# Performance work log

Measured on AMD Instinct MI355X. Metric: run time of the kernel, lower is better.

## Reference

```python
import jax, jax.numpy as jnp
import numpy as np

IN_DIM = 1024
FF = 512
OUT = 128
TEMP = 1.0  # temperature=1 passed in __init__
EPS = 1e-5  # BatchNorm3d eps


def make_pe(n, d):
    # PositionalEncoding table, rows 0..n-1
    pos = jnp.arange(n, dtype=jnp.float32)[:, None]
    div = jnp.exp(jnp.arange(0, d, 2, dtype=jnp.float32) * (-np.log(10000.0) / d))
    ang = pos * div  # [n, d/2]
    return jnp.stack([jnp.sin(ang), jnp.cos(ang)], axis=-1).reshape(n, d)


def _nonlocal(x, kw, qw, vw, ow, ob, g, beta):
    # x: [B, C, T, H, W]; 1x1x1 convs are channel matmuls
    B, C, T, H, W = x.shape
    K = jnp.einsum('bcthw,fc->bfthw', x, kw).reshape(B, FF, -1)
    Q = jnp.einsum('bcthw,fc->bfthw', x, qw).reshape(B, FF, -1)
    V = jnp.einsum('bcthw,fc->bfthw', x, vw).reshape(B, FF, -1)
    KQ = jnp.einsum('bcn,bcm->bnm', K, Q)  # K^T Q over channels -> [B,N,N]
    attn = jax.nn.softmax(KQ / TEMP, axis=2)
    # torch: sum_j V[b,c,n] * attn[b,n,j]  == V * attn.sum(axis=2)
    Vo = (V * attn.sum(axis=2)[:, None, :]).reshape(B, FF, T, H, W)
    o = jnp.einsum('bfthw,of->bothw', Vo, ow) + ob[None, :, None, None, None]
    y = x + jax.nn.relu(o)
    # BatchNorm3d, training-mode batch statistics over (B,T,H,W)
    m = y.mean(axis=(0, 2, 3, 4))
    v = y.var(axis=(0, 2, 3, 4))
    inv = jax.lax.rsqrt(v + EPS)
    return ((y - m[None, :, None, None, None]) * inv[None, :, None, None, None]
            * g[None, :, None, None, None] + beta[None, :, None, None, None])


def _convt2(x, w, b):
    # ConvTranspose2d(kernel=2, stride=2): each input pixel emits a 2x2 block
    B, C, H, W = x.shape
    y = jnp.einsum('bchw,cokl->bohkwl', x, w).reshape(B, w.shape[1], 2 * H, 2 * W)
    return y + b[None, :, None, None]


def setup_inputs() -> dict:
    key = jax.random.key(0)
    ks = jax.random.split(key, 32)
    n = lambda k, s, sc: jax.random.normal(k, s, dtype=jnp.float32) * sc
    d = {
        'context': n(ks[0], (4, 4, IN_DIM, 16, 16), 1.0),
        'frame': n(ks[1], (4, 6, IN_DIM, 8, 8), 1.0),
    }
    i = 2
    for l in (0, 1):
        d[f'nl{l}_kw'] = n(ks[i], (FF, IN_DIM), IN_DIM ** -0.5); i += 1
        d[f'nl{l}_qw'] = n(ks[i], (FF, IN_DIM), IN_DIM ** -0.5); i += 1
        d[f'nl{l}_vw'] = n(ks[i], (FF, IN_DIM), IN_DIM ** -0.5); i += 1
        d[f'nl{l}_ow'] = n(ks[i], (IN_DIM, FF), FF ** -0.5); i += 1
        d[f'nl{l}_ob'] = n(ks[i], (IN_DIM,), 0.02); i += 1
        d[f'nl{l}_g'] = jnp.ones((IN_DIM,), jnp.float32)
        d[f'nl{l}_beta'] = jnp.zeros((IN_DIM,), jnp.float32)
    d['tp_w'] = n(ks[i], (FF, IN_DIM, 3, 3, 3), (IN_DIM * 27) ** -0.5); i += 1
    d['tp_b'] = n(ks[i], (FF,), 0.02); i += 1
    d['up1_w'] = n(ks[i], (IN_DIM, FF, 2, 2), IN_DIM ** -0.5); i += 1
    d['up1_b'] = n(ks[i], (FF,), 0.02); i += 1
    d['up2_w'] = n(ks[i], (FF, FF, 2, 2), FF ** -0.5); i += 1
    d['up2_b'] = n(ks[i], (FF,), 0.02); i += 1
    for p in ('og', 'os'):
        d[f'{p}1_w'] = n(ks[i], (FF, FF), FF ** -0.5); i += 1
        d[f'{p}1_b'] = n(ks[i], (FF,), 0.02); i += 1
        d[f'{p}2_w'] = n(ks[i], (OUT, FF), FF ** -0.5); i += 1
        d[f'{p}2_b'] = n(ks[i], (OUT,), 0.02); i += 1
    return d


def reference(context, frame,
              nl0_kw, nl0_qw, nl0_vw, nl0_ow, nl0_ob, nl0_g, nl0_beta,
              nl1_kw, nl1_qw, nl1_vw, nl1_ow, nl1_ob, nl1_g, nl1_beta,
              tp_w, tp_b, up1_w, up1_b, up2_w, up2_b,
              og1_w, og1_b, og2_w, og2_b, os1_w, os1_b, os2_w, os2_b):
    # context: [B, Tc, C, H, W] -> [B, C, Tc, H, W]
    x = jnp.transpose(context, (0, 2, 1, 3, 4))
    x = _nonlocal(x, nl0_kw, nl0_qw, nl0_vw, nl0_ow, nl0_ob, nl0_g, nl0_beta)
    x = _nonlocal(x, nl1_kw, nl1_qw, nl1_vw, nl1_ow, nl1_ob, nl1_g, nl1_beta)
    # temporal pool: Conv3d kernel 3, VALID, then ReLU and global avg pool
    tp = jax.lax.conv_general_dilated(x, tp_w, (1, 1, 1), 'VALID',
                                      dimension_numbers=('NCDHW', 'OIDHW', 'NCDHW'))
    tp = jax.nn.relu(tp + tp_b[None, :, None, None, None])
    goal_pre = tp.mean(axis=(2, 3, 4))  # [B, FF]
    B, T, C, H, W = frame.shape
    f = frame.reshape(B * T, C, H, W)
    s = jax.nn.relu(_convt2(f, up1_w, up1_b))
    s = _convt2(s, up2_w, up2_b)  # [B*T, FF, 4H, 4W]
    Ns = 16 * H * W
    se = s.reshape(B * T, FF, Ns)
    pe = make_pe(Ns, FF)
    Vt = jnp.transpose(se, (0, 2, 1)) + pe[None]  # [B*T, Ns, FF]
    goal_rep = jnp.repeat(goal_pre, T, axis=0)  # [B*T, FF]
    SG = jnp.einsum('bcn,bc->bn', se, goal_rep)
    attn = jax.nn.softmax(SG / TEMP, axis=1)
    sga = jnp.einsum('bn,bnc->bc', attn, Vt).reshape(B, T, FF)
    goal = jax.nn.relu(goal_pre @ og1_w.T + og1_b) @ og2_w.T + og2_b
    state = jax.nn.relu(sga @ os1_w.T + os1_b) @ os2_w.T + os2_b
    return goal, state
```

## Files before the change

kernel.cpp:

```cpp
#include <hip/hip_runtime.h>
#include <hip/hip_bf16.h>

using bf16 = __hip_bfloat16;
typedef short short8 __attribute__((ext_vector_type(8)));
typedef float float4v __attribute__((ext_vector_type(4)));

__device__ __forceinline__ float b2f(unsigned short u){
  unsigned int x = ((unsigned int)u) << 16; float f;
  __builtin_memcpy(&f, &x, 4); return f;
}
__device__ __forceinline__ float b2f(bf16 v){ return __bfloat162float(v); }
__device__ __forceinline__ unsigned short f2bu(float x){
  bf16 h = __float2bfloat16(x); unsigned short u;
  __builtin_memcpy(&u, &h, 2); return u;
}

#define GLDS16(g, l) __builtin_amdgcn_global_load_lds( \
    (const __attribute__((address_space(1))) void*)(g), \
    (__attribute__((address_space(3))) void*)(l), 16, 0, 0)

template<class TO>
__launch_bounds__(256)
__global__ void permT_k(const float* __restrict__ inp, TO* __restrict__ outp,
                        int Cc, int R, int D, int G, long inS, long outS){
  __shared__ float t[64][65];
  int z = blockIdx.z;
  const float* in = inp + (size_t)z*inS;
  TO* out = outp + (size_t)z*outS;
  int c0 = blockIdx.x*64, r0 = blockIdx.y*64;
  int tid = threadIdx.x;
  int rr = tid>>2, c4 = (tid&3)*16;
  const float* p = in + (size_t)(r0+rr)*Cc + c0 + c4;
  #pragma unroll
  for (int j=0;j<16;j+=4){
    float4 q = *reinterpret_cast<const float4*>(p+j);
    t[rr][c4+j]=q.x; t[rr][c4+j+1]=q.y; t[rr][c4+j+2]=q.z; t[rr][c4+j+3]=q.w;
  }
  __syncthreads();
  int ql = tid>>2;
  int q = c0 + ql;
  int orow = (q % D)*G + q / D;
  TO* op = out + (size_t)orow*R + r0 + c4;
  #pragma unroll
  for (int j=0;j<16;j++){
    if constexpr (sizeof(TO)==2) op[j] = __float2bfloat16(t[c4+j][ql]);
    else op[j] = t[c4+j][ql];
  }
}

template<int PAT>
__launch_bounds__(256)
__global__ void permTsplit3_k(const float* __restrict__ inp, unsigned short* __restrict__ outp,
                              int Cc, int R, int D, int G, long inS, long outS){
  __shared__ float t[64][65];
  int z = blockIdx.z;
  const float* in = inp + (size_t)z*inS;
  unsigned short* out = outp + (size_t)z*outS;
  int c0 = blockIdx.x*64, r0 = blockIdx.y*64;
  int tid = threadIdx.x;
  int rr = tid>>2, c4 = (tid&3)*16;
  const float* p = in + (size_t)(r0+rr)*Cc + c0 + c4;
  #pragma unroll
  for (int j=0;j<16;j+=4){
    float4 q = *reinterpret_cast<const float4*>(p+j);
    t[rr][c4+j]=q.x; t[rr][c4+j+1]=q.y; t[rr][c4+j+2]=q.z; t[rr][c4+j+3]=q.w;
  }
  __syncthreads();
  int ql = tid>>2;
  int q = c0 + ql;
  int orow = (q % D)*G + q / D;
  unsigned short* op = out + (size_t)orow*(3*R);
  #pragma unroll
  for (int j=0;j<16;j++){
    float v = t[c4+j][ql];
    unsigned short h = f2bu(v);
    unsigned short l = f2bu(v - b2f(h));
    int idx = r0 + c4 + j;
    if constexpr (PAT==0){
      op[idx] = h; op[R+idx] = l; op[2*R+idx] = h;
    } else {
      op[idx] = h; op[R+idx] = h; op[2*R+idx] = l;
    }
  }
}

__launch_bounds__(256)
__global__ void splitA_k(const float* __restrict__ in, unsigned short* __restrict__ out){
  int idx = blockIdx.x*256 + threadIdx.x;
  int m = idx >> 9, j = idx & 511;
  float v = in[idx];
  unsigned short h = f2bu(v);
  unsigned short l = f2bu(v - b2f(h));
  unsigned short* op = out + (size_t)m*1536 + j;
  op[0] = h; op[512] = l; op[1024] = h;
}

__global__ void zero_k(float* __restrict__ p){
  p[blockIdx.x*256 + threadIdx.x] = 0.f;
}

template<int WM, int WN, int MTM, int NTN, int MODE, int BK>
__launch_bounds__(256)
__global__ void mmL_k(const unsigned short* __restrict__ A,
                      const unsigned short* __restrict__ B,
                      const float* __restrict__ bias,
                      const unsigned short* __restrict__ res,
                      const float* __restrict__ gpf,
                      float* __restrict__ outf,
                      unsigned short* __restrict__ outs,
                      float* __restrict__ aux,
                      int K){
  constexpr int BM  = WM*MTM*16;
  constexpr int BN  = WN*NTN*16;
  constexpr int CPR = BK/8;
  constexpr int KS  = BK/32;
  constexpr int AIT = (BM*CPR)/256;
  constexpr int NBC = (BN*CPR)/256;
  constexpr int LPT = AIT + NBC;
  __shared__ __align__(16) short As[2*BM*BK];
  __shared__ __align__(16) short Bs[2*BN*BK];
  const int tid = threadIdx.x;
  const int wv = tid>>6, lane = tid&63, l15 = lane&15, quad = lane>>4;
  const int wvm = wv / WN, wvf = wv % WN;
  const int wbase = wv<<6;

  int bx = blockIdx.x, by = blockIdx.y, bz = blockIdx.z;
  if constexpr (MODE==1){
    const int gx = gridDim.x, gy = gridDim.y, gz = gridDim.z;
    const int n = gx*gy*gz;
    const int lin = bx + gx*(by + gy*bz);
    const int q = n >> 3, r = n & 7;
    const int xcd = lin & 7, j = lin >> 3;
    const int work = (xcd < r ? xcd*(q+1) : r*(q+1) + (xcd-r)*q) + j;
    by = work % gy;
    const int t = work / gy;
    bx = t % gx;
    bz = t / gx;
  }
  const int m0 = bx*BM;
  const int fblk = by*BN;
  const int z = bz;

  auto swz = [](int row){ if constexpr (BK==32) return (row>>1)&3; else return row&7; };

  size_t aAddr[AIT];
  #pragma unroll
  for (int it=0; it<AIT; ++it){
    int s = tid + it*256;
    int arow = s/CPR;
    int ac = (s&(CPR-1)) ^ swz(arow);
    int m = m0 + arow;
    if constexpr (MODE==1){
      int mm = m < 1568 ? m : 1567;
      int b = mm/392, r = mm%392;
      int t = r/196, r2 = r%196;
      int hh = r2/14, ww = r2%14;
      int kt = z/3, kh = z%3;
      int sp = ((b*4 + t + kt)*16 + hh + kh)*16 + ww;
      aAddr[it] = (size_t)sp*1024 + ac*8;
    } else {
      aAddr[it] = (size_t)m*K + ac*8;
    }
  }
  size_t bAddr[NBC];
  #pragma unroll
  for (int it=0; it<NBC; ++it){
    int s = tid + it*256;
    int row = s/CPR;
    int c = (s&(CPR-1)) ^ swz(row);
    int f = fblk + row;
    if constexpr (MODE==0)      bAddr[it] = (size_t)f*1024 + c*8;
    else if constexpr (MODE==1) bAddr[it] = (size_t)f*27648 + (size_t)z*3072 + c*8;
    else                        bAddr[it] = ((size_t)z*512 + f)*(size_t)K + c*8;
  }
  int aslot[MTM][KS];
  #pragma unroll
  for (int mt=0;mt<MTM;++mt)
    #pragma unroll
    for (int ks=0;ks<KS;++ks){
      int row = wvm*MTM*16 + mt*16 + l15;
      aslot[mt][ks] = row*CPR + ((ks*4 + quad) ^ swz(row));
    }
  int bslot[NTN][KS];
  #pragma unroll
  for (int nt=0;nt<NTN;++nt)
    #pragma unroll
    for (int ks=0;ks<KS;++ks){
      int row = wvf*NTN*16 + nt*16 + l15;
      bslot[nt][ks] = row*CPR + ((ks*4 + quad) ^ swz(row));
    }

  float4v acc[MTM][NTN];
  #pragma unroll
  for (int i=0;i<MTM;i++)
    #pragma unroll
    for (int j=0;j<NTN;j++) acc[i][j]=(float4v){0,0,0,0};

  auto stage = [&](int buf, int k0){
    #pragma unroll
    for (int it=0; it<AIT; ++it)
      GLDS16(A + aAddr[it] + k0, As + buf*(BM*BK) + (it*256 + wbase)*8);
    #pragma unroll
    for (int it=0; it<NBC; ++it)
      GLDS16(B + bAddr[it] + k0, Bs + buf*(BN*BK) + (it*256 + wbase)*8);
  };
  auto computeTile = [&](int buf){
    const short* ap = As + buf*(BM*BK);
    const short* bp = Bs + buf*(BN*BK);
    #pragma unroll
    for (int ks=0; ks<KS; ++ks){
      short8 bf[NTN];
      #pragma unroll
      for (int nt=0;nt<NTN;++nt)
        bf[nt] = *reinterpret_cast<const short8*>(bp + bslot[nt][ks]*8);
      #pragma unroll
      for (int mt=0;mt<MTM;++mt){
        short8 af = *reinterpret_cast<const short8*>(ap + aslot[mt][ks]*8);
        #pragma unroll
        for (int nt=0;nt<NTN;++nt)
          acc[mt][nt] = __builtin_amdgcn_mfma_f32_16x16x32_bf16(af, bf[nt], acc[mt][nt],0,0,0);
      }
    }
  };

  stage(0, 0);
  int cur = 0;
  for (int k0 = 0; k0 < K-BK; k0 += BK){
    stage(cur^1, k0+BK);
    if constexpr (LPT==8)      asm volatile("s_waitcnt vmcnt(8)" ::: "memory");
    else if constexpr (LPT==6) asm volatile("s_waitcnt vmcnt(6)" ::: "memory");
    else if constexpr (LPT==5) asm volatile("s_waitcnt vmcnt(5)" ::: "memory");
    else if constexpr (LPT==4) asm volatile("s_waitcnt vmcnt(4)" ::: "memory");
    else                       asm volatile("s_waitcnt vmcnt(3)" ::: "memory");
    __builtin_amdgcn_sched_barrier(0);
    __builtin_amdgcn_s_barrier();
    computeTile(cur);
    asm volatile("s_waitcnt lgkmcnt(0)" ::: "memory");
    __builtin_amdgcn_sched_barrier(0);
    __builtin_amdgcn_s_barrier();
    cur ^= 1;
  }
  asm volatile("s_waitcnt vmcnt(0)" ::: "memory");
  __builtin_amdgcn_sched_barrier(0);
  __builtin_amdgcn_s_barrier();
  computeTile(cur);

  if constexpr (MODE==0){
    const float* badd = outf;
    float sacc[NTN] = {}, s2acc[NTN] = {};
    #pragma unroll
    for (int nt=0;nt<NTN;++nt){
      int f = fblk + wvf*NTN*16 + nt*16 + l15;
      float bi = bias[f] + (badd ? badd[f] : 0.f);
      float rsc = 1.f, rsh = 0.f;
      if (gpf){ rsc = gpf[f]; rsh = gpf[1024+f]; }
      #pragma unroll
      for (int mt=0;mt<MTM;++mt){
        #pragma unroll
        for (int r=0;r<4;++r){
          int m = m0 + wvm*MTM*16 + mt*16 + quad*4 + r;
          float v = fmaxf(acc[mt][nt][r]+bi, 0.f) + b2f(res[(size_t)m*1024 + f])*rsc + rsh;
          outs[(size_t)m*1024 + f] = f2bu(v);
          sacc[nt] += v; s2acc[nt] += v*v;
        }
      }
    }
    #pragma unroll
    for (int nt=0;nt<NTN;++nt){
      float s = sacc[nt], s2 = s2acc[nt];
      s  += __shfl_xor(s, 16);  s  += __shfl_xor(s, 32);
      s2 += __shfl_xor(s2, 16); s2 += __shfl_xor(s2, 32);
      if (quad==0){
        int f = fblk + wvf*NTN*16 + nt*16 + l15;
        aux[(size_t)bx*2048 + f] = s;
        aux[(size_t)bx*2048 + 1024 + f] = s2;
      }
    }
  } else if constexpr (MODE==1){
    #pragma unroll
    for (int mt=0;mt<MTM;++mt)
      #pragma unroll
      for (int nt=0;nt<NTN;++nt){
        int f = fblk + wvf*NTN*16 + nt*16 + l15;
        #pragma unroll
        for (int r=0;r<4;++r){
          int m = m0 + wvm*MTM*16 + mt*16 + quad*4 + r;
          if (m < 1568) outf[((size_t)z*1568 + m)*512 + f] = acc[mt][nt][r];
        }
      }
  } else if constexpr (MODE==2){
    int kk = z>>1, ll = z&1;
    #pragma unroll
    for (int mt=0;mt<MTM;++mt)
      #pragma unroll
      for (int nt=0;nt<NTN;++nt){
        int f = fblk + wvf*NTN*16 + nt*16 + l15;
        float bi = bias[f];
        #pragma unroll
        for (int r=0;r<4;++r){
          int m = m0 + wvm*MTM*16 + mt*16 + quad*4 + r;
          int bt = m>>6, p = m&63;
          long orow = (long)bt*256 + (2*(p>>3)+kk)*16 + 2*(p&7)+ll;
          float v = fmaxf(acc[mt][nt][r]+bi, 0.f);
          unsigned short h = f2bu(v);
          unsigned short l = f2bu(v - b2f(h));
          unsigned short* rp = outs + (size_t)orow*1536 + f;
          rp[0] = h; rp[512] = l; rp[1024] = h;
        }
      }
  } else if constexpr (MODE==5){
    int kk = z>>1, ll = z&1;
    #pragma unroll
    for (int mt=0;mt<MTM;++mt){
      int mbase = m0 + wvm*MTM*16 + mt*16;
      int bt = mbase>>8, b6 = bt/6, p0 = mbase&255;
      float gv[NTN], bv[NTN];
      #pragma unroll
      for (int nt=0;nt<NTN;++nt){
        int f = fblk + wvf*NTN*16 + nt*16 + l15;
        gv[nt] = gpf[b6*512 + f];
        bv[nt] = bias[f];
      }
      #pragma unroll
      for (int r=0;r<4;++r){
        int p = p0 + quad*4 + r;
        long orow = (long)bt*1024 + (2*(p>>4)+kk)*32 + 2*(p&15)+ll;
        float sdot = 0.f;
        #pragma unroll
        for (int nt=0;nt<NTN;++nt){
          int f = fblk + wvf*NTN*16 + nt*16 + l15;
          float v = acc[mt][nt][r] + bv[nt];
          outf[(size_t)orow*512 + f] = v;
          sdot += v * gv[nt];
        }
        sdot += __shfl_xor(sdot, 1); sdot += __shfl_xor(sdot, 2);
        sdot += __shfl_xor(sdot, 4); sdot += __shfl_xor(sdot, 8);
        if (l15==0) atomicAdd(aux + orow, sdot);
      }
    }
  } else {
    if (gpf){
      float sc[NTN], sh[NTN];
      #pragma unroll
      for (int nt=0;nt<NTN;++nt){
        int f = fblk + wvf*NTN*16 + nt*16 + l15;
        sc[nt] = gpf[f]; sh[nt] = gpf[1024+f];
      }
      #pragma unroll
      for (int mt=0;mt<MTM;++mt){
        #pragma unroll
        for (int r=0;r<4;++r){
          int m = m0 + wvm*MTM*16 + mt*16 + quad*4 + r;
          float part = 0.f;
          #pragma unroll
          for (int nt=0;nt<NTN;++nt){
            int f = fblk + wvf*NTN*16 + nt*16 + l15;
            float a = acc[mt][nt][r];
            part += a * sh[nt];
            outs[(size_t)m*1024 + f] = f2bu(a * sc[nt]);
          }
          part += __shfl_xor(part, 1); part += __shfl_xor(part, 2);
          part += __shfl_xor(part, 4); part += __shfl_xor(part, 8);
          if (l15==0) atomicAdd(aux + m, part);
        }
      }
    } else {
      #pragma unroll
      for (int mt=0;mt<MTM;++mt)
        #pragma unroll
        for (int nt=0;nt<NTN;++nt){
          int f = fblk + wvf*NTN*16 + nt*16 + l15;
          #pragma unroll
          for (int r=0;r<4;++r){
            int m = m0 + wvm*MTM*16 + mt*16 + quad*4 + r;
            outs[(size_t)m*1024 + f] = f2bu(acc[mt][nt][r]);
          }
        }
    }
  }
}

__global__ void stats_comb(const float* __restrict__ bnp, const float* __restrict__ g,
                           const float* __restrict__ beta, float* __restrict__ mv){
  int c = blockIdx.x*256 + threadIdx.x;
  float S=0.f, S2=0.f;
  #pragma unroll 8
  for (int s=0;s<64;s++){ S += bnp[(size_t)s*2048 + c]; S2 += bnp[(size_t)s*2048 + 1024 + c]; }
  float m = S * (1.f/4096.f);
  float var = S2 * (1.f/4096.f) - m*m;
  float inv = rsqrtf(var + 1e-5f);
  float sc = inv * g[c];
  mv[c] = sc;
  mv[1024 + c] = beta[c] - m*sc;
}

__launch_bounds__(256)
__global__ void wperm_k(const float* __restrict__ w, const float* __restrict__ mv1,
                        unsigned short* __restrict__ wtt, float* __restrict__ tpb2){
  __shared__ float ls[3456];
  __shared__ float rs[256];
  int f = blockIdx.x, cc = blockIdx.y;
  const float* src = w + (size_t)f*27648 + cc*3456;
  unsigned short* dst = wtt + (size_t)f*27648;
  for (int i=threadIdx.x; i<3456; i+=256) ls[i] = src[i];
  __syncthreads();
  float part = 0.f;
  for (int u=threadIdx.x; u<3456; u+=256){
    int j = u >> 7, c = u & 127;
    int ch = cc*128 + c;
    float wv = ls[c*27 + j];
    dst[(size_t)j*1024 + ch] = f2bu(wv * mv1[ch]);
    part += wv * mv1[1024 + ch];
  }
  rs[threadIdx.x] = part; __syncthreads();
  for (int st=128; st>0; st>>=1){
    if (threadIdx.x < st) rs[threadIdx.x] += rs[threadIdx.x+st];
    __syncthreads();
  }
  if (threadIdx.x==0) atomicAdd(tpb2 + f, rs[0]);
}

__launch_bounds__(256)
__global__ void gp2_k(const float* __restrict__ part9, const float* __restrict__ tpb,
                      const float* __restrict__ tpbA, float* __restrict__ gp){
  int b = blockIdx.x;
  int fc = blockIdx.y;
  int z = blockIdx.z;
  int fi = threadIdx.x & 31, pi = threadIdx.x >> 5;
  int f = fc*32 + fi;
  float bias = tpb[f] + tpbA[f];
  float a = 0.f;
  for (int p = z*98 + pi; p < z*98 + 98; p += 8){
    size_t base = ((size_t)(b*392 + p))*512 + f;
    float v = bias;
    #pragma unroll
    for (int i=0;i<9;i++) v += part9[(size_t)i*802816 + base];
    a += fmaxf(v, 0.f);
  }
  __shared__ float red[256];
  red[threadIdx.x] = a; __syncthreads();
  for (int st=4; st>0; st>>=1){
    if (pi < st) red[pi*32+fi] += red[(pi+st)*32+fi];
    __syncthreads();
  }
  if (pi==0) atomicAdd(gp + b*512 + f, red[fi] * (1.f/392.f));
}

__global__ void pen_k(float* __restrict__ peN){
  int idx = blockIdx.x*256 + threadIdx.x;
  int n = idx >> 9, c = idx & 511;
  float div = expf(-0.035977892f * (float)(c>>1));
  float ang = (float)n * div;
  peN[idx] = (c & 1) ? cosf(ang) : sinf(ang);
}

__launch_bounds__(256)
__global__ void softmax_k(const float* __restrict__ SG, float* __restrict__ attn){
  int bt = blockIdx.x; int tid = threadIdx.x;
  float4 v = *reinterpret_cast<const float4*>(SG + bt*1024 + tid*4);
  float mx = fmaxf(fmaxf(v.x,v.y), fmaxf(v.z,v.w));
  __shared__ float red[256];
  red[tid] = mx; __syncthreads();
  for (int st=128; st>0; st>>=1){
    if (tid<st) red[tid] = fmaxf(red[tid], red[tid+st]);
    __syncthreads();
  }
  float m = red[0]; __syncthreads();
  float4 e;
  e.x = expf(v.x-m); e.y = expf(v.y-m); e.z = expf(v.z-m); e.w = expf(v.w-m);
  red[tid] = e.x+e.y+e.z+e.w; __syncthreads();
  for (int st=128; st>0; st>>=1){
    if (tid<st) red[tid] += red[tid+st];
    __syncthreads();
  }
  float inv = 1.0f/red[0];
  e.x*=inv; e.y*=inv; e.z*=inv; e.w*=inv;
  *reinterpret_cast<float4*>(attn + bt*1024 + tid*4) = e;
}

__launch_bounds__(256)
__global__ void sga2_k(const float* __restrict__ scl, const float* __restrict__ peN,
                       const float* __restrict__ attn, float* __restrict__ sga){
  int bt = blockIdx.x, sl = blockIdx.y;
  int tid = threadIdx.x;
  __shared__ float at[128];
  if (tid < 128) at[tid] = attn[bt*1024 + sl*128 + tid];
  __syncthreads();
  float acc0 = 0.f, acc1 = 0.f;
  for (int j=0;j<128;j++){
    int n = sl*128 + j;
    float a = at[j];
    const float* row = scl + ((size_t)bt*1024 + n)*512;
    const float* pe  = peN + (size_t)n*512;
    acc0 += a * (row[tid] + pe[tid]);
    acc1 += a * (row[tid+256] + pe[tid+256]);
  }
  atomicAdd(sga + (size_t)bt*512 + tid, acc0);
  atomicAdd(sga + (size_t)bt*512 + 256 + tid, acc1);
}

__launch_bounds__(256)
__global__ void mlp_k(const float* __restrict__ in, const float* __restrict__ w1,
                      const float* __restrict__ b1, const float* __restrict__ w2,
                      const float* __restrict__ b2, float* __restrict__ out){
  int bb = blockIdx.x; int tid = threadIdx.x;
  __shared__ float xv[512]; __shared__ float h[512];
  xv[tid] = in[(size_t)bb*512 + tid];
  xv[tid+256] = in[(size_t)bb*512 + 256 + tid];
  __syncthreads();
  #pragma unroll
  for (int oo=0;oo<2;oo++){
    int o = tid + oo*256;
    const float* wr = w1 + (size_t)o*512;
    float a=0.f;
    for (int c=0;c<512;c+=4){
      float4 q = *reinterpret_cast<const float4*>(wr+c);
      a += xv[c]*q.x + xv[c+1]*q.y + xv[c+2]*q.z + xv[c+3]*q.w;
    }
    h[o] = fmaxf(a + b1[o], 0.f);
  }
  __syncthreads();
  if (tid < 128){
    const float* wr = w2 + (size_t)tid*512;
    float a=0.f;
    for (int c=0;c<512;c+=4){
      float4 q = *reinterpret_cast<const float4*>(wr+c);
      a += h[c]*q.x + h[c+1]*q.y + h[c+2]*q.z + h[c+3]*q.w;
    }
    out[(size_t)bb*128+tid] = a + b2[tid];
  }
}

extern "C" void kernel_launch(void* const* d_in, const int* in_sizes, int n_in,
                              void* d_out, int out_size, void* d_ws, size_t ws_size,
                              hipStream_t stream){
  (void)in_sizes; (void)n_in; (void)out_size; (void)ws_size;
  const float* ctx   = (const float*)d_in[0];
  const float* frame = (const float*)d_in[1];
  const float* nl_vw[2] = {(const float*)d_in[4],  (const float*)d_in[11]};
  const float* nl_ow[2] = {(const float*)d_in[5],  (const float*)d_in[12]};
  const float* nl_ob[2] = {(const float*)d_in[6],  (const float*)d_in[13]};
  const float* nl_g[2]  = {(const float*)d_in[7],  (const float*)d_in[14]};
  const float* nl_be[2] = {(const float*)d_in[8],  (const float*)d_in[15]};
  const float* tp_w = (const float*)d_in[16]; const float* tp_b = (const float*)d_in[17];
  const float* up1w = (const float*)d_in[18]; const float* up1b = (const float*)d_in[19];
  const float* up2w = (const float*)d_in[20]; const float* up2b = (const float*)d_in[21];
  const float* og1w = (const float*)d_in[22]; const float* og1b = (const float*)d_in[23];
  const float* og2w = (const float*)d_in[24]; const float* og2b = (const float*)d_in[25];
  const float* os1w = (const float*)d_in[26]; const float* os1b = (const float*)d_in[27];
  const float* os2w = (const float*)d_in[28]; const float* os2b = (const float*)d_in[29];
  float* out = (float*)d_out;

  char* wsp = (char*)d_ws;
  float* bias2   = (float*)(wsp + 65536);
  float* tpb2    = (float*)(wsp + 69632);
  float* gp      = (float*)(wsp + 73728);
  float* mv0     = (float*)(wsp + 131072);
  float* mv1     = (float*)(wsp + 139264);
  float* SG      = (float*)(wsp + 147456);
  float* attn    = (float*)(wsp + 245760);
  float* sga     = (float*)(wsp + 344064);
  float* peN     = (float*)(wsp + 786432);
  bf16*  weff    = (bf16*) (wsp + 2883584);
  unsigned short* w1sp = (unsigned short*)(wsp + 4980736);
  unsigned short* w2sp = (unsigned short*)(wsp + 17563648);
  char* ov = wsp + 23855104;
  bf16*  xclA = (bf16*) (ov);
  bf16*  xclB = (bf16*) (ov + 8388608);
  unsigned short* Asp = (unsigned short*)(ov + 36700160);
  unsigned short* Bsp = (unsigned short*)(ov + 36700160 + 3145728);
  float* bnp = (float*)(ov + 36700160 + 6291456);
  unsigned short* wtt = (unsigned short*)(ov + 8388608);
  float* part9 = (float*)(ov + 36700160);
  unsigned short* Fsp = (unsigned short*)(ov + 36700160);
  unsigned short* s1sp = (unsigned short*)(ov);
  float* scl  = (float*)(ov + 18874368);

  permT_k<bf16><<<dim3(4,16,16),256,0,stream>>>(ctx, xclA, 256, 1024, 1, 1, 262144L, 262144L);
  permTsplit3_k<1><<<dim3(32,16,1),256,0,stream>>>(up1w, w1sp, 2048, 1024, 4, 512, 0L, 0L);
  permTsplit3_k<1><<<dim3(32,8,1),256,0,stream>>>(up2w, w2sp, 2048, 512, 4, 512, 0L, 0L);
  pen_k<<<2048,256,0,stream>>>(peN);
  zero_k<<<320,256,0,stream>>>((float*)(wsp + 65536));

  splitA_k<<<2048,256,0,stream>>>(nl_ow[0], Asp);
  permTsplit3_k<1><<<dim3(16,8,1),256,0,stream>>>(nl_vw[0], Bsp, 1024, 512, 1, 1, 0L, 0L);
  mmL_k<1,4,2,2,4,64><<<dim3(32,8,1),256,0,stream>>>(Asp, Bsp, nullptr, nullptr, nullptr,
      nullptr, (unsigned short*)weff, nullptr, 1536);
  mmL_k<1,4,4,2,0,64><<<dim3(64,8,1),256,0,stream>>>((const unsigned short*)xclA,
      (const unsigned short*)weff, nl_ob[0], (const unsigned short*)xclA, nullptr,
      nullptr, (unsigned short*)xclB, bnp, 1024);
  stats_comb<<<4,256,0,stream>>>(bnp, nl_g[0], nl_be[0], mv0);

  splitA_k<<<2048,256,0,stream>>>(nl_ow[1], Asp);
  permTsplit3_k<1><<<dim3(16,8,1),256,0,stream>>>(nl_vw[1], Bsp, 1024, 512, 1, 1, 0L, 0L);
  mmL_k<1,4,2,2,4,64><<<dim3(32,8,1),256,0,stream>>>(Asp, Bsp, nullptr, nullptr, mv0,
      nullptr, (unsigned short*)weff, bias2, 1536);
  mmL_k<1,4,4,2,0,64><<<dim3(64,8,1),256,0,stream>>>((const unsigned short*)xclB,
      (const unsigned short*)weff, nl_ob[1], (const unsigned short*)xclB, mv0,
      bias2, (unsigned short*)xclA, bnp, 1024);
  stats_comb<<<4,256,0,stream>>>(bnp, nl_g[1], nl_be[1], mv1);

  wperm_k<<<dim3(512,8),256,0,stream>>>(tp_w, mv1, wtt, tpb2);
  mmL_k<2,2,4,4,1,64><<<dim3(13,4,9),256,0,stream>>>((const unsigned short*)xclA, wtt,
      nullptr, nullptr, nullptr, part9, nullptr, nullptr, 3072);
  gp2_k<<<dim3(4,16,4),256,0,stream>>>(part9, tp_b, tpb2, gp);

  permTsplit3_k<0><<<dim3(1,16,24),256,0,stream>>>(frame, Fsp, 64, 1024, 1, 1, 65536L, 196608L);
  mmL_k<1,4,2,2,2,64><<<dim3(48,4,4),256,0,stream>>>(Fsp, w1sp, up1b, nullptr, nullptr,
      nullptr, s1sp, nullptr, 3072);
  mmL_k<2,2,4,4,5,32><<<dim3(48,4,4),256,0,stream>>>(s1sp, w2sp, up2b, nullptr, gp,
      scl, nullptr, SG, 1536);

  softmax_k<<<24,256,0,stream>>>(SG, attn);
  sga2_k<<<dim3(24,8),256,0,stream>>>(scl, peN, attn, sga);

  mlp_k<<<4,256,0,stream>>>(gp, og1w, og1b, og2w, og2b, out);
  mlp_k<<<24,256,0,stream>>>(sga, os1w, os1b, os2w, os2b, out + 512);
}
```

Measured before the change: 617.0 us.

## Triple-buffer GEMM LDS pipeline and retune tile and split sizes

The bf16 MFMA GEMM goes from double to triple buffering of its LDS tiles. This drops the second barrier and the lgkmcnt wait per K step, so a buffer is only refilled two iterations after it was consumed. Several launch shapes also change: BK=32 for the temporal-pool GEMM, a taller M tile for the first up-conv GEMM, and finer splits for the gp2 reduction (8 z slices) and the sga2 weighted sum (32 slices, with more atomics). The triple buffering raises LDS use per block, which may lower occupancy.

```diff
diff --git a/kernel.cpp b/kernel.cpp
--- a/kernel.cpp
+++ b/kernel.cpp
@@ -18,6 +18,17 @@
 #define GLDS16(g, l) __builtin_amdgcn_global_load_lds( \
     (const __attribute__((address_space(1))) void*)(g), \
     (__attribute__((address_space(3))) void*)(l), 16, 0, 0)
+
+template<int N> __device__ __forceinline__ void vwait(){
+  if constexpr (N==0)       asm volatile("s_waitcnt vmcnt(0)" ::: "memory");
+  else if constexpr (N==3)  asm volatile("s_waitcnt vmcnt(3)" ::: "memory");
+  else if constexpr (N==4)  asm volatile("s_waitcnt vmcnt(4)" ::: "memory");
+  else if constexpr (N==5)  asm volatile("s_waitcnt vmcnt(5)" ::: "memory");
+  else if constexpr (N==6)  asm volatile("s_waitcnt vmcnt(6)" ::: "memory");
+  else if constexpr (N==8)  asm volatile("s_waitcnt vmcnt(8)" ::: "memory");
+  else if constexpr (N==10) asm volatile("s_waitcnt vmcnt(10)" ::: "memory");
+  else                      asm volatile("s_waitcnt vmcnt(12)" ::: "memory");
+}
 
 template<class TO>
 __launch_bounds__(256)
@@ -117,8 +128,8 @@
   constexpr int AIT = (BM*CPR)/256;
   constexpr int NBC = (BN*CPR)/256;
   constexpr int LPT = AIT + NBC;
-  __shared__ __align__(16) short As[2*BM*BK];
-  __shared__ __align__(16) short Bs[2*BN*BK];
+  __shared__ __align__(16) short As[3*BM*BK];
+  __shared__ __align__(16) short Bs[3*BN*BK];
   const int tid = threadIdx.x;
   const int wv = tid>>6, lane = tid&63, l15 = lane&15, quad = lane>>4;
   const int wvm = wv / WN, wvf = wv % WN;
@@ -223,34 +234,30 @@
     }
   };
 
-  stage(0, 0);
-  int cur = 0;
-  for (int k0 = 0; k0 < K-BK; k0 += BK){
-    stage(cur^1, k0+BK);
-    if constexpr (LPT==8)      asm volatile("s_waitcnt vmcnt(8)" ::: "memory");
-    else if constexpr (LPT==6) asm volatile("s_waitcnt vmcnt(6)" ::: "memory");
-    else if constexpr (LPT==5) asm volatile("s_waitcnt vmcnt(5)" ::: "memory");
-    else if constexpr (LPT==4) asm volatile("s_waitcnt vmcnt(4)" ::: "memory");
-    else                       asm volatile("s_waitcnt vmcnt(3)" ::: "memory");
+  const int nt = K/BK;
+  int b0=0, b1=1, b2=2;
+  stage(b0, 0);
+  for (int t=0; t<nt-1; ++t){
+    stage(b1, (t+1)*BK);
+    vwait<LPT>();
     __builtin_amdgcn_sched_barrier(0);
     __builtin_amdgcn_s_barrier();
-    computeTile(cur);
-    asm volatile("s_waitcnt lgkmcnt(0)" ::: "memory");
     __builtin_amdgcn_sched_barrier(0);
-    __builtin_amdgcn_s_barrier();
-    cur ^= 1;
-  }
-  asm volatile("s_waitcnt vmcnt(0)" ::: "memory");
+    computeTile(b0);
+    int tmp=b0; b0=b1; b1=b2; b2=tmp;
+  }
+  vwait<0>();
   __builtin_amdgcn_sched_barrier(0);
   __builtin_amdgcn_s_barrier();
-  computeTile(cur);
+  __builtin_amdgcn_sched_barrier(0);
+  computeTile(b0);
 
   if constexpr (MODE==0){
     const float* badd = outf;
     float sacc[NTN] = {}, s2acc[NTN] = {};
     #pragma unroll
-    for (int nt=0;nt<NTN;++nt){
-      int f = fblk + wvf*NTN*16 + nt*16 + l15;
+    for (int nt2=0;nt2<NTN;++nt2){
+      int f = fblk + wvf*NTN*16 + nt2*16 + l15;
       float bi = bias[f] + (badd ? badd[f] : 0.f);
       float rsc = 1.f, rsh = 0.f;
       if (gpf){ rsc = gpf[f]; rsh = gpf[1024+f]; }
@@ -259,19 +266,19 @@
         #pragma unroll
         for (int r=0;r<4;++r){
           int m = m0 + wvm*MTM*16 + mt*16 + quad*4 + r;
-          float v = fmaxf(acc[mt][nt][r]+bi, 0.f) + b2f(res[(size_t)m*1024 + f])*rsc + rsh;
+          float v = fmaxf(acc[mt][nt2][r]+bi, 0.f) + b2f(res[(size_t)m*1024 + f])*rsc + rsh;
           outs[(size_t)m*1024 + f] = f2bu(v);
-          sacc[nt] += v; s2acc[nt] += v*v;
+          sacc[nt2] += v; s2acc[nt2] += v*v;
         }
       }
     }
     #pragma unroll
-    for (int nt=0;nt<NTN;++nt){
-      float s = sacc[nt], s2 = s2acc[nt];
+    for (int nt2=0;nt2<NTN;++nt2){
+      float s = sacc[nt2], s2 = s2acc[nt2];
       s  += __shfl_xor(s, 16);  s  += __shfl_xor(s, 32);
       s2 += __shfl_xor(s2, 16); s2 += __shfl_xor(s2, 32);
       if (quad==0){
-        int f = fblk + wvf*NTN*16 + nt*16 + l15;
+        int f = fblk + wvf*NTN*16 + nt2*16 + l15;
         aux[(size_t)bx*2048 + f] = s;
         aux[(size_t)bx*2048 + 1024 + f] = s2;
       }
@@ -280,12 +287,12 @@
     #pragma unroll
     for (int mt=0;mt<MTM;++mt)
       #pragma unroll
-      for (int nt=0;nt<NTN;++nt){
-        int f = fblk + wvf*NTN*16 + nt*16 + l15;
+      for (int nt2=0;nt2<NTN;++nt2){
+        int f = fblk + wvf*NTN*16 + nt2*16 + l15;
         #pragma unroll
         for (int r=0;r<4;++r){
           int m = m0 + wvm*MTM*16 + mt*16 + quad*4 + r;
-          if (m < 1568) outf[((size_t)z*1568 + m)*512 + f] = acc[mt][nt][r];
+          if (m < 1568) outf[((size_t)z*1568 + m)*512 + f] = acc[mt][nt2][r];
         }
       }
   } else if constexpr (MODE==2){
@@ -293,15 +300,15 @@
     #pragma unroll
     for (int mt=0;mt<MTM;++mt)
       #pragma unroll
-      for (int nt=0;nt<NTN;++nt){
-        int f = fblk + wvf*NTN*16 + nt*16 + l15;
+      for (int nt2=0;nt2<NTN;++nt2){
+        int f = fblk + wvf*NTN*16 + nt2*16 + l15;
         float bi = bias[f];
         #pragma unroll
         for (int r=0;r<4;++r){
           int m = m0 + wvm*MTM*16 + mt*16 + quad*4 + r;
           int bt = m>>6, p = m&63;
           long orow = (long)bt*256 + (2*(p>>3)+kk)*16 + 2*(p&7)+ll;
-          float v = fmaxf(acc[mt][nt][r]+bi, 0.f);
+          float v = fmaxf(acc[mt][nt2][r]+bi, 0.f);
           unsigned short h = f2bu(v);
           unsigned short l = f2bu(v - b2f(h));
           unsigned short* rp = outs + (size_t)orow*1536 + f;
@@ -316,10 +323,10 @@
       int bt = mbase>>8, b6 = bt/6, p0 = mbase&255;
       float gv[NTN], bv[NTN];
       #pragma unroll
-      for (int nt=0;nt<NTN;++nt){
-        int f = fblk + wvf*NTN*16 + nt*16 + l15;
-        gv[nt] = gpf[b6*512 + f];
-        bv[nt] = bias[f];
+      for (int nt2=0;nt2<NTN;++nt2){
+        int f = fblk + wvf*NTN*16 + nt2*16 + l15;
+        gv[nt2] = gpf[b6*512 + f];
+        bv[nt2] = bias[f];
       }
       #pragma unroll
       for (int r=0;r<4;++r){
@@ -327,11 +334,11 @@
         long orow = (long)bt*1024 + (2*(p>>4)+kk)*32 + 2*(p&15)+ll;
         float sdot = 0.f;
         #pragma unroll
-        for (int nt=0;nt<NTN;++nt){
-          int f = fblk + wvf*NTN*16 + nt*16 + l15;
-          float v = acc[mt][nt][r] + bv[nt];
+        for (int nt2=0;nt2<NTN;++nt2){
+          int f = fblk + wvf*NTN*16 + nt2*16 + l15;
+          float v = acc[mt][nt2][r] + bv[nt2];
           outf[(size_t)orow*512 + f] = v;
-          sdot += v * gv[nt];
+          sdot += v * gv[nt2];
         }
         sdot += __shfl_xor(sdot, 1); sdot += __shfl_xor(sdot, 2);
         sdot += __shfl_xor(sdot, 4); sdot += __shfl_xor(sdot, 8);
@@ -342,9 +349,9 @@
     if (gpf){
       float sc[NTN], sh[NTN];
       #pragma unroll
-      for (int nt=0;nt<NTN;++nt){
-        int f = fblk + wvf*NTN*16 + nt*16 + l15;
-        sc[nt] = gpf[f]; sh[nt] = gpf[1024+f];
+      for (int nt2=0;nt2<NTN;++nt2){
+        int f = fblk + wvf*NTN*16 + nt2*16 + l15;
+        sc[nt2] = gpf[f]; sh[nt2] = gpf[1024+f];
       }
       #pragma unroll
       for (int mt=0;mt<MTM;++mt){
@@ -353,11 +360,11 @@
           int m = m0 + wvm*MTM*16 + mt*16 + quad*4 + r;
           float part = 0.f;
           #pragma unroll
-          for (int nt=0;nt<NTN;++nt){
-            int f = fblk + wvf*NTN*16 + nt*16 + l15;
-            float a = acc[mt][nt][r];
-            part += a * sh[nt];
-            outs[(size_t)m*1024 + f] = f2bu(a * sc[nt]);
+          for (int nt2=0;nt2<NTN;++nt2){
+            int f = fblk + wvf*NTN*16 + nt2*16 + l15;
+            float a = acc[mt][nt2][r];
+            part += a * sh[nt2];
+            outs[(size_t)m*1024 + f] = f2bu(a * sc[nt2]);
           }
           part += __shfl_xor(part, 1); part += __shfl_xor(part, 2);
           part += __shfl_xor(part, 4); part += __shfl_xor(part, 8);
@@ -368,12 +375,12 @@
       #pragma unroll
       for (int mt=0;mt<MTM;++mt)
         #pragma unroll
-        for (int nt=0;nt<NTN;++nt){
-          int f = fblk + wvf*NTN*16 + nt*16 + l15;
+        for (int nt2=0;nt2<NTN;++nt2){
+          int f = fblk + wvf*NTN*16 + nt2*16 + l15;
           #pragma unroll
           for (int r=0;r<4;++r){
             int m = m0 + wvm*MTM*16 + mt*16 + quad*4 + r;
-            outs[(size_t)m*1024 + f] = f2bu(acc[mt][nt][r]);
+            outs[(size_t)m*1024 + f] = f2bu(acc[mt][nt2][r]);
           }
         }
     }
@@ -430,7 +437,7 @@
   int f = fc*32 + fi;
   float bias = tpb[f] + tpbA[f];
   float a = 0.f;
-  for (int p = z*98 + pi; p < z*98 + 98; p += 8){
+  for (int p = z*49 + pi; p < z*49 + 49; p += 8){
     size_t base = ((size_t)(b*392 + p))*512 + f;
     float v = bias;
     #pragma unroll
@@ -483,12 +490,12 @@
                        const float* __restrict__ attn, float* __restrict__ sga){
   int bt = blockIdx.x, sl = blockIdx.y;
   int tid = threadIdx.x;
-  __shared__ float at[128];
-  if (tid < 128) at[tid] = attn[bt*1024 + sl*128 + tid];
+  __shared__ float at[32];
+  if (tid < 32) at[tid] = attn[bt*1024 + sl*32 + tid];
   __syncthreads();
   float acc0 = 0.f, acc1 = 0.f;
-  for (int j=0;j<128;j++){
-    int n = sl*128 + j;
+  for (int j=0;j<32;j++){
+    int n = sl*32 + j;
     float a = at[j];
     const float* row = scl + ((size_t)bt*1024 + n)*512;
     const float* pe  = peN + (size_t)n*512;
@@ -601,18 +608,18 @@
   stats_comb<<<4,256,0,stream>>>(bnp, nl_g[1], nl_be[1], mv1);
 
   wperm_k<<<dim3(512,8),256,0,stream>>>(tp_w, mv1, wtt, tpb2);
-  mmL_k<2,2,4,4,1,64><<<dim3(13,4,9),256,0,stream>>>((const unsigned short*)xclA, wtt,
+  mmL_k<2,2,4,4,1,32><<<dim3(13,4,9),256,0,stream>>>((const unsigned short*)xclA, wtt,
       nullptr, nullptr, nullptr, part9, nullptr, nullptr, 3072);
-  gp2_k<<<dim3(4,16,4),256,0,stream>>>(part9, tp_b, tpb2, gp);
+  gp2_k<<<dim3(4,16,8),256,0,stream>>>(part9, tp_b, tpb2, gp);
 
   permTsplit3_k<0><<<dim3(1,16,24),256,0,stream>>>(frame, Fsp, 64, 1024, 1, 1, 65536L, 196608L);
-  mmL_k<1,4,2,2,2,64><<<dim3(48,4,4),256,0,stream>>>(Fsp, w1sp, up1b, nullptr, nullptr,
+  mmL_k<1,4,4,2,2,64><<<dim3(24,4,4),256,0,stream>>>(Fsp, w1sp, up1b, nullptr, nullptr,
       nullptr, s1sp, nullptr, 3072);
   mmL_k<2,2,4,4,5,32><<<dim3(48,4,4),256,0,stream>>>(s1sp, w2sp, up2b, nullptr, gp,
       scl, nullptr, SG, 1536);
 
   softmax_k<<<24,256,0,stream>>>(SG, attn);
-  sga2_k<<<dim3(24,8),256,0,stream>>>(scl, peN, attn, sga);
+  sga2_k<<<dim3(24,32),256,0,stream>>>(scl, peN, attn, sga);
 
   mlp_k<<<4,256,0,stream>>>(gp, og1w, og1b, og2w, og2b, out);
   mlp_k<<<24,256,0,stream>>>(sga, os1w, os1b, os2w, os2b, out + 512);
```

New measurement: 602.8 us. -2.3%, faster.
